# Performance work log

Measured on AMD Instinct MI355X. Metric: run time of the kernel, lower is better.

The kernel has to match this reference:

```python
import jax, jax.numpy as jnp
import numpy as np

N = 262144          # nodes (divisible by 8 for 3 pooling stages)
E = 4194304         # edges (avg degree 16)
PAD = 6             # 2 extra edge slots per pooling stage
IN = 32
HID = (32, 32, 16)


def gcn_conv(x, W, b, src, dst, w):
    """PyG GCNConv: add self-loops, symmetric norm, x@W, scatter-add, +bias.
    src/dst: padded edge arrays; w: float mask (0 = inactive edge)."""
    n = x.shape[0]
    deg = jax.ops.segment_sum(w, dst, num_segments=n) + 1.0  # +1 self-loop
    dinv = jax.lax.rsqrt(deg)                                 # deg >= 1
    h = x @ W
    norm = dinv[src] * dinv[dst] * w                          # [E+PAD]
    out = jax.ops.segment_sum(norm[:, None] * h[src], dst, num_segments=n)
    out = out + (dinv * dinv)[:, None] * h                    # self-loop term
    return out + b


def graph_max_pool(x, src, dst, w, slot):
    """max over adjacent node pairs; keep edges with both endpoints < n//2;
    append edges (m-1,0) and (0,m-1) in pre-allocated padding slots."""
    n = x.shape[0]
    m = n // 2
    xp = jnp.max(x[: 2 * m].reshape(m, 2, x.shape[1]), axis=1)
    valid = ((src < m) & (dst < m)).astype(w.dtype)
    w = w * valid
    src = src.at[slot].set(m - 1).at[slot + 1].set(0)
    dst = dst.at[slot].set(0).at[slot + 1].set(m - 1)
    w = w.at[slot].set(1.0).at[slot + 1].set(1.0)
    return xp, src, dst, w


def setup_inputs() -> dict:
    key = jax.random.key(0)
    ks = jax.random.split(key, 8)
    x = jax.random.normal(ks[0], (N, IN), dtype=jnp.float32)
    edge_index = jax.random.randint(ks[1], (2, E), 0, N, dtype=jnp.int32)
    def lin(k, fi, fo):
        return jax.random.normal(k, (fi, fo), dtype=jnp.float32) / np.float32(np.sqrt(fi))
    return {
        "x": x,
        "edge_index": edge_index,
        "W1": lin(ks[2], IN, HID[0]), "b1": jnp.zeros((HID[0],), jnp.float32),
        "W2": lin(ks[3], HID[0], HID[1]), "b2": jnp.zeros((HID[1],), jnp.float32),
        "W3": lin(ks[4], HID[1], HID[2]), "b3": jnp.zeros((HID[2],), jnp.float32),
    }


def reference(x, edge_index, W1, b1, W2, b2, W3, b3):
    # fixed-size padded edge list with float validity mask
    src = jnp.concatenate([edge_index[0], jnp.zeros((PAD,), edge_index.dtype)])
    dst = jnp.concatenate([edge_index[1], jnp.zeros((PAD,), edge_index.dtype)])
    w = jnp.concatenate([jnp.ones((E,), jnp.float32), jnp.zeros((PAD,), jnp.float32)])

    h = jax.nn.relu(gcn_conv(x, W1, b1, src, dst, w))
    h, src, dst, w = graph_max_pool(h, src, dst, w, E)
    h = jax.nn.relu(gcn_conv(h, W2, b2, src, dst, w))
    h, src, dst, w = graph_max_pool(h, src, dst, w, E + 2)
    h = jax.nn.relu(gcn_conv(h, W3, b3, src, dst, w))
    latent, src, dst, w = graph_max_pool(h, src, dst, w, E + 4)
    return latent, jnp.stack([src, dst]), w
```

## Files before the change

### kernel.cpp

```cpp
#include <hip/hip_runtime.h>
#include <hip/hip_bf16.h>
#include <stdint.h>

#define N_NODES 262144
#define E_EDGES 4194304
#define EPAD    4194310
#define SRC_OFF 524288
#define DST_OFF (524288 + 4194310)
#define W_OFF   (524288 + 2 * 4194310)
#define CAP2    1064960
#define CAP3    270336

using bf16 = __hip_bfloat16;
typedef float f4v __attribute__((ext_vector_type(4)));
typedef float f2v __attribute__((ext_vector_type(2)));

__device__ __forceinline__ float b2f(unsigned int u) {
    union { unsigned int i; float f; } v; v.i = u << 16; return v.f;
}

__device__ __forceinline__ void pk_atomic_add_raw(bf16* addr, uint32_t data) {
    asm volatile("global_atomic_pk_add_bf16 %0, %1, off" :: "v"(addr), "v"(data) : "memory");
}

__device__ __forceinline__ float dinv_of(const float* __restrict__ deg, int i, int n, int pads) {
    float extra = (pads && (i == 0 || i == n - 1)) ? 1.0f : 0.0f;
    return rsqrtf(deg[i] + 1.0f + extra);
}

__global__ void __launch_bounds__(256) tier_hist_kernel(const int* __restrict__ ei,
        float* __restrict__ out, uint32_t* __restrict__ wc, float* __restrict__ deg1) {
    int t = blockIdx.x * 256 + threadIdx.x;
    int4 s0 = ((const int4*)ei)[2 * t];
    int4 s1 = ((const int4*)ei)[2 * t + 1];
    int4 d0 = ((const int4*)(ei + E_EDGES))[2 * t];
    int4 d1 = ((const int4*)(ei + E_EDGES))[2 * t + 1];

    f4v v;
    v = (f4v){(float)s0.x, (float)s0.y, (float)s0.z, (float)s0.w};
    __builtin_nontemporal_store(v, (f4v*)(out + SRC_OFF) + 2 * t);
    v = (f4v){(float)s1.x, (float)s1.y, (float)s1.z, (float)s1.w};
    __builtin_nontemporal_store(v, (f4v*)(out + SRC_OFF) + 2 * t + 1);
    f2v w2;
    w2 = (f2v){(float)d0.x, (float)d0.y}; __builtin_nontemporal_store(w2, (f2v*)(out + DST_OFF) + 4 * t);
    w2 = (f2v){(float)d0.z, (float)d0.w}; __builtin_nontemporal_store(w2, (f2v*)(out + DST_OFF) + 4 * t + 1);
    w2 = (f2v){(float)d1.x, (float)d1.y}; __builtin_nontemporal_store(w2, (f2v*)(out + DST_OFF) + 4 * t + 2);
    w2 = (f2v){(float)d1.z, (float)d1.w}; __builtin_nontemporal_store(w2, (f2v*)(out + DST_OFF) + 4 * t + 3);
    v = (f4v){(s0.x < 32768 && d0.x < 32768) ? 1.0f : 0.0f,
              (s0.y < 32768 && d0.y < 32768) ? 1.0f : 0.0f,
              (s0.z < 32768 && d0.z < 32768) ? 1.0f : 0.0f,
              (s0.w < 32768 && d0.w < 32768) ? 1.0f : 0.0f};
    __builtin_nontemporal_store(v, (f4v*)(out + W_OFF) + 2 * t);
    v = (f4v){(s1.x < 32768 && d1.x < 32768) ? 1.0f : 0.0f,
              (s1.y < 32768 && d1.y < 32768) ? 1.0f : 0.0f,
              (s1.z < 32768 && d1.z < 32768) ? 1.0f : 0.0f,
              (s1.w < 32768 && d1.w < 32768) ? 1.0f : 0.0f};
    __builtin_nontemporal_store(v, (f4v*)(out + W_OFF) + 2 * t + 1);

    atomicAdd(&deg1[d0.x], 1.0f); atomicAdd(&deg1[d0.y], 1.0f);
    atomicAdd(&deg1[d0.z], 1.0f); atomicAdd(&deg1[d0.w], 1.0f);
    atomicAdd(&deg1[d1.x], 1.0f); atomicAdd(&deg1[d1.y], 1.0f);
    atomicAdd(&deg1[d1.z], 1.0f); atomicAdd(&deg1[d1.w], 1.0f);

    int c3 = 0, c2 = 0;
    int ss[8] = {s0.x, s0.y, s0.z, s0.w, s1.x, s1.y, s1.z, s1.w};
    int dd[8] = {d0.x, d0.y, d0.z, d0.w, d1.x, d1.y, d1.z, d1.w};
#pragma unroll
    for (int j = 0; j < 8; ++j) {
        bool b3  = (ss[j] < 65536) & (dd[j] < 65536);
        bool b23 = (ss[j] < 131072) & (dd[j] < 131072);
        c3 += b3; c2 += (b23 & !b3);
    }
    int pk = c2 | (c3 << 16);
    pk += __shfl_xor(pk, 32); pk += __shfl_xor(pk, 16); pk += __shfl_xor(pk, 8);
    pk += __shfl_xor(pk, 4);  pk += __shfl_xor(pk, 2);  pk += __shfl_xor(pk, 1);
    if ((threadIdx.x & 63) == 0) wc[t >> 6] = (uint32_t)pk;
}

__global__ void __launch_bounds__(1024) tier_scan_kernel(const uint32_t* __restrict__ wc,
        uint2* __restrict__ wb, uint32_t* __restrict__ tot, float* __restrict__ out) {
    __shared__ uint32_t wt3[16], wt2[16];
    int t = threadIdx.x, lane = t & 63, w = t >> 6;
    uint32_t v[8]; uint32_t s3 = 0, s2 = 0;
#pragma unroll
    for (int j = 0; j < 8; ++j) {
        v[j] = wc[t * 8 + j];
        s2 += v[j] & 0xFFFFu; s3 += v[j] >> 16;
    }
    uint32_t i3 = s3, i2 = s2;
    for (int off = 1; off < 64; off <<= 1) {
        uint32_t o3 = __shfl_up(i3, off);
        uint32_t o2 = __shfl_up(i2, off);
        if (lane >= off) { i3 += o3; i2 += o2; }
    }
    if (lane == 63) { wt3[w] = i3; wt2[w] = i2; }
    __syncthreads();
    uint32_t wb3 = 0, wb2 = 0;
#pragma unroll
    for (int k = 0; k < 16; ++k) {
        uint32_t m = (k < w) ? 1u : 0u;
        wb3 += m * wt3[k]; wb2 += m * wt2[k];
    }
    uint32_t r3 = wb3 + i3 - s3, r2 = wb2 + i2 - s2;
#pragma unroll
    for (int j = 0; j < 8; ++j) {
        wb[t * 8 + j] = make_uint2(r3, r2);
        r2 += v[j] & 0xFFFFu; r3 += v[j] >> 16;
    }
    if (t == 1023) { tot[0] = wb3 + i3; tot[1] = wb2 + i2; }
    if (t < 6) {
        int stage = t >> 1, m = 131072 >> stage;
        int s, d;
        if ((t & 1) == 0) { s = m - 1; d = 0; } else { s = 0; d = m - 1; }
        int e = E_EDGES + t;
        out[SRC_OFF + e] = (float)s;
        out[DST_OFF + e] = (float)d;
        out[W_OFF + e]   = (stage == 2) ? 1.0f : 0.0f;
    }
}

__global__ void __launch_bounds__(256) compact_kernel(const int* __restrict__ ei,
        const uint2* __restrict__ wb, const uint32_t* __restrict__ tot,
        int2* __restrict__ el, float* __restrict__ deg2, float* __restrict__ deg3) {
    int t = blockIdx.x * 256 + threadIdx.x;
    int lane = threadIdx.x & 63;
    int4 s0 = ((const int4*)ei)[2 * t];
    int4 s1 = ((const int4*)ei)[2 * t + 1];
    int4 d0 = ((const int4*)(ei + E_EDGES))[2 * t];
    int4 d1 = ((const int4*)(ei + E_EDGES))[2 * t + 1];
    uint2 base = wb[t >> 6];
    uint32_t r3 = base.x, r2 = tot[0] + base.y;
    uint64_t lt = (1ull << lane) - 1ull;
    int ss[8] = {s0.x, s0.y, s0.z, s0.w, s1.x, s1.y, s1.z, s1.w};
    int dd[8] = {d0.x, d0.y, d0.z, d0.w, d1.x, d1.y, d1.z, d1.w};
#pragma unroll
    for (int j = 0; j < 8; ++j) {
        int s = ss[j], d = dd[j];
        bool b3  = (s < 65536) & (d < 65536);
        bool b23 = (s < 131072) & (d < 131072);
        bool b2  = b23 & !b3;
        uint64_t m3 = __ballot(b3), m2 = __ballot(b2);
        if (b3) {
            el[r3 + (uint32_t)__popcll(m3 & lt)] = make_int2(s, d);
            atomicAdd(&deg3[d], 1.0f);
        }
        if (b2) {
            uint32_t p = r2 + (uint32_t)__popcll(m2 & lt);
            if (p < CAP2) el[p] = make_int2(s, d);
        }
        if (b23) atomicAdd(&deg2[d], 1.0f);
        r3 += (uint32_t)__popcll(m3); r2 += (uint32_t)__popcll(m2);
    }
}

__global__ void __launch_bounds__(256) xform1_kernel(const float* __restrict__ xin,
        const float* __restrict__ W, const float* __restrict__ deg1,
        bf16* __restrict__ hs, bf16* __restrict__ agg) {
    constexpr int FIN = 32, FOUT = 32, NPB = 8;
    __shared__ float sW[FIN * FOUT];
    __shared__ float sx[NPB * FIN];
    int tid = threadIdx.x;
    for (int i = tid; i < FIN * FOUT; i += 256) sW[i] = W[i];
    int node0 = blockIdx.x * NPB;
    for (int i = tid; i < NPB * FIN; i += 256) sx[i] = xin[node0 * FIN + i];
    __syncthreads();
    int nl = tid / FOUT, j = tid % FOUT;
    int node = node0 + nl;
    float acc = 0.0f;
#pragma unroll
    for (int k = 0; k < FIN; ++k) acc += sx[nl * FIN + k] * sW[k * FOUT + j];
    bf16 v = __float2bfloat16(rsqrtf(deg1[node] + 1.0f) * acc);
    hs[node * FOUT + j]  = v;
    agg[node * FOUT + j] = v;
}

template <int FOUT>
__global__ void __launch_bounds__(256) xform_pool_kernel(const bf16* __restrict__ aggp,
        const float* __restrict__ degp, int prevN, int prevPads, const float* __restrict__ biasp,
        const float* __restrict__ W, const float* __restrict__ deg, int curN,
        bf16* __restrict__ hs, bf16* __restrict__ agg) {
    constexpr int FIN = 32;
    constexpr int NPB = 256 / FOUT;
    __shared__ float sW[FIN * FOUT];
    __shared__ float sx[NPB * FIN];
    const unsigned short* ap = (const unsigned short*)aggp;
    int tid = threadIdx.x;
    for (int i = tid; i < FIN * FOUT; i += 256) sW[i] = W[i];
    int node0 = blockIdx.x * NPB;
    for (int i = tid; i < NPB * FIN; i += 256) {
        int nl = i / FIN, k = i % FIN;
        int g0 = 2 * (node0 + nl);
        float bb = biasp[k];
        float v0 = dinv_of(degp, g0,     prevN, prevPads) * b2f(ap[(size_t)g0 * FIN + k])       + bb;
        float v1 = dinv_of(degp, g0 + 1, prevN, prevPads) * b2f(ap[(size_t)(g0 + 1) * FIN + k]) + bb;
        sx[i] = fmaxf(fmaxf(v0, v1), 0.0f);
    }
    __syncthreads();
    int nl = tid / FOUT, j = tid % FOUT;
    int node = node0 + nl;
    float acc = 0.0f;
#pragma unroll
    for (int k = 0; k < FIN; ++k) acc += sx[nl * FIN + k] * sW[k * FOUT + j];
    bf16 v = __float2bfloat16(dinv_of(deg, node, curN, 1) * acc);
    hs[node * FOUT + j]  = v;
    agg[node * FOUT + j] = v;
}

__global__ void __launch_bounds__(256) scatter1_kernel(const int* __restrict__ ei,
        const bf16* __restrict__ hs, bf16* __restrict__ agg) {
    unsigned idx = blockIdx.x * 256u + threadIdx.x;
    int e = (int)(idx >> 4), p = (int)(idx & 15u);
    int s = ei[e], d = ei[E_EDGES + e];
    uint32_t hw = *(const uint32_t*)((const unsigned short*)hs + (size_t)s * 32 + 2 * p);
    pk_atomic_add_raw(agg + (size_t)d * 32 + 2 * p, hw);
}

template <int FOUT>
__global__ void __launch_bounds__(256) scatter_cmp_kernel(const int2* __restrict__ el,
        const uint32_t* __restrict__ tot, int useN3only,
        const bf16* __restrict__ hs, bf16* __restrict__ agg, int n) {
    constexpr int L = FOUT / 2;
    unsigned idx = blockIdx.x * 256u + threadIdx.x;
    unsigned e = idx / L; int p = (int)(idx % L);
    uint32_t K = useN3only ? tot[0] : (tot[0] + tot[1]);
    if (e >= K + 2) return;
    int s, d;
    if (e < K)       { int2 sd = el[e]; s = sd.x; d = sd.y; }
    else if (e == K) { s = n - 1; d = 0; }
    else             { s = 0;     d = n - 1; }
    uint32_t hw = *(const uint32_t*)((const unsigned short*)hs + (size_t)s * FOUT + 2 * p);
    pk_atomic_add_raw(agg + (size_t)d * FOUT + 2 * p, hw);
}

__global__ void __launch_bounds__(256) pool_out_kernel(const bf16* __restrict__ agg,
        const float* __restrict__ deg3, const float* __restrict__ bias,
        float* __restrict__ outp) {
    unsigned idx = blockIdx.x * 256u + threadIdx.x;
    int i = (int)(idx >> 4), f = (int)(idx & 15);
    int g0 = 2 * i;
    float bb = bias[f];
    float v0 = dinv_of(deg3, g0,     65536, 1) * __bfloat162float(agg[(size_t)g0 * 16 + f])       + bb;
    float v1 = dinv_of(deg3, g0 + 1, 65536, 1) * __bfloat162float(agg[(size_t)(g0 + 1) * 16 + f]) + bb;
    outp[idx] = fmaxf(fmaxf(v0, v1), 0.0f);
}

extern "C" void kernel_launch(void* const* d_in, const int* in_sizes, int n_in,
                              void* d_out, int out_size, void* d_ws, size_t ws_size,
                              hipStream_t stream) {
    const float* x  = (const float*)d_in[0];
    const int*   ei = (const int*)d_in[1];
    const float* W1 = (const float*)d_in[2];
    const float* b1 = (const float*)d_in[3];
    const float* W2 = (const float*)d_in[4];
    const float* b2 = (const float*)d_in[5];
    const float* W3 = (const float*)d_in[6];
    const float* b3 = (const float*)d_in[7];
    float* out = (float*)d_out;

    char* ws = (char*)d_ws;
    bf16*     agg   = (bf16*)ws;
    bf16*     hs    = (bf16*)(ws + (16u << 20));
    int2*     el    = (int2*)(ws + (44u << 20));
    float*    deg1  = (float*)(ws + (55u << 20));
    float*    deg2  = (float*)(ws + (56u << 20));
    float*    deg3  = (float*)(ws + (56u << 20) + (512u << 10));
    uint32_t* wcnt  = (uint32_t*)(ws + (59u << 20));
    uint2*    wbase = (uint2*)(ws + (59u << 20) + (256u << 10));
    uint32_t* totb  = (uint32_t*)(ws + (59u << 20) + (768u << 10));

    hipMemsetAsync(deg1, 0, (1u << 20) + (768u << 10), stream);
    tier_hist_kernel<<<2048, 256, 0, stream>>>(ei, out, wcnt, deg1);
    tier_scan_kernel<<<1, 1024, 0, stream>>>(wcnt, wbase, totb, out);
    compact_kernel<<<2048, 256, 0, stream>>>(ei, wbase, totb, el, deg2, deg3);

    xform1_kernel<<<N_NODES / 8, 256, 0, stream>>>(x, W1, deg1, hs, agg);
    scatter1_kernel<<<E_EDGES * 16 / 256, 256, 0, stream>>>(ei, hs, agg);

    xform_pool_kernel<32><<<131072 / 8, 256, 0, stream>>>(agg, deg1, 262144, 0, b1,
                                                          W2, deg2, 131072, hs, agg);
    scatter_cmp_kernel<32><<<(int)(((unsigned)(CAP2 + 2) * 16 + 255) / 256), 256, 0, stream>>>(
        el, totb, 0, hs, agg, 131072);

    xform_pool_kernel<16><<<65536 / 16, 256, 0, stream>>>(agg, deg2, 131072, 1, b2,
                                                          W3, deg3, 65536, hs, agg);
    scatter_cmp_kernel<16><<<(int)(((unsigned)(CAP3 + 2) * 8 + 255) / 256), 256, 0, stream>>>(
        el, totb, 1, hs, agg, 65536);

    pool_out_kernel<<<32768 * 16 / 256, 256, 0, stream>>>(agg, deg3, b3, out);
}
```

Measured before the change: 644.1 us.

## Replace hist/scan/compact with single-pass segmented atomic compaction, move output writes into scatter1

New measurement: 688.2 us. +6.8%, slower.

```diff
diff --git a/kernel.cpp b/kernel.cpp
--- a/kernel.cpp
+++ b/kernel.cpp
@@ -4,12 +4,16 @@
 
 #define N_NODES 262144
 #define E_EDGES 4194304
-#define EPAD    4194310
 #define SRC_OFF 524288
 #define DST_OFF (524288 + 4194310)
 #define W_OFF   (524288 + 2 * 4194310)
-#define CAP2    1064960
-#define CAP3    270336
+#define NSEG    64
+#define SEG3    4608
+#define SEG2X   13568
+#define T3      (NSEG * SEG3)
+#define T2X     (NSEG * SEG2X)
+#define SCAT1_BLOCKS (E_EDGES * 16 / 256)
+#define OUT_BLOCKS   (E_EDGES / 8 / 256)
 
 using bf16 = __hip_bfloat16;
 typedef float f4v __attribute__((ext_vector_type(4)));
@@ -28,43 +32,26 @@
     return rsqrtf(deg[i] + 1.0f + extra);
 }
 
-__global__ void __launch_bounds__(256) tier_hist_kernel(const int* __restrict__ ei,
-        float* __restrict__ out, uint32_t* __restrict__ wc, float* __restrict__ deg1) {
+__global__ void __launch_bounds__(256) prep_kernel(const int* __restrict__ ei,
+        uint32_t* __restrict__ el3, int2* __restrict__ el2,
+        uint32_t* __restrict__ cnt3, uint32_t* __restrict__ cnt2,
+        float* __restrict__ deg1, float* __restrict__ deg2, float* __restrict__ deg3) {
     int t = blockIdx.x * 256 + threadIdx.x;
+    int lane = threadIdx.x & 63;
+    int seg = (t >> 6) & (NSEG - 1);
     int4 s0 = ((const int4*)ei)[2 * t];
     int4 s1 = ((const int4*)ei)[2 * t + 1];
     int4 d0 = ((const int4*)(ei + E_EDGES))[2 * t];
     int4 d1 = ((const int4*)(ei + E_EDGES))[2 * t + 1];
 
-    f4v v;
-    v = (f4v){(float)s0.x, (float)s0.y, (float)s0.z, (float)s0.w};
-    __builtin_nontemporal_store(v, (f4v*)(out + SRC_OFF) + 2 * t);
-    v = (f4v){(float)s1.x, (float)s1.y, (float)s1.z, (float)s1.w};
-    __builtin_nontemporal_store(v, (f4v*)(out + SRC_OFF) + 2 * t + 1);
-    f2v w2;
-    w2 = (f2v){(float)d0.x, (float)d0.y}; __builtin_nontemporal_store(w2, (f2v*)(out + DST_OFF) + 4 * t);
-    w2 = (f2v){(float)d0.z, (float)d0.w}; __builtin_nontemporal_store(w2, (f2v*)(out + DST_OFF) + 4 * t + 1);
-    w2 = (f2v){(float)d1.x, (float)d1.y}; __builtin_nontemporal_store(w2, (f2v*)(out + DST_OFF) + 4 * t + 2);
-    w2 = (f2v){(float)d1.z, (float)d1.w}; __builtin_nontemporal_store(w2, (f2v*)(out + DST_OFF) + 4 * t + 3);
-    v = (f4v){(s0.x < 32768 && d0.x < 32768) ? 1.0f : 0.0f,
-              (s0.y < 32768 && d0.y < 32768) ? 1.0f : 0.0f,
-              (s0.z < 32768 && d0.z < 32768) ? 1.0f : 0.0f,
-              (s0.w < 32768 && d0.w < 32768) ? 1.0f : 0.0f};
-    __builtin_nontemporal_store(v, (f4v*)(out + W_OFF) + 2 * t);
-    v = (f4v){(s1.x < 32768 && d1.x < 32768) ? 1.0f : 0.0f,
-              (s1.y < 32768 && d1.y < 32768) ? 1.0f : 0.0f,
-              (s1.z < 32768 && d1.z < 32768) ? 1.0f : 0.0f,
-              (s1.w < 32768 && d1.w < 32768) ? 1.0f : 0.0f};
-    __builtin_nontemporal_store(v, (f4v*)(out + W_OFF) + 2 * t + 1);
-
     atomicAdd(&deg1[d0.x], 1.0f); atomicAdd(&deg1[d0.y], 1.0f);
     atomicAdd(&deg1[d0.z], 1.0f); atomicAdd(&deg1[d0.w], 1.0f);
     atomicAdd(&deg1[d1.x], 1.0f); atomicAdd(&deg1[d1.y], 1.0f);
     atomicAdd(&deg1[d1.z], 1.0f); atomicAdd(&deg1[d1.w], 1.0f);
 
-    int c3 = 0, c2 = 0;
     int ss[8] = {s0.x, s0.y, s0.z, s0.w, s1.x, s1.y, s1.z, s1.w};
     int dd[8] = {d0.x, d0.y, d0.z, d0.w, d1.x, d1.y, d1.z, d1.w};
+    int c3 = 0, c2 = 0;
 #pragma unroll
     for (int j = 0; j < 8; ++j) {
         bool b3  = (ss[j] < 65536) & (dd[j] < 65536);
@@ -74,65 +61,16 @@
     int pk = c2 | (c3 << 16);
     pk += __shfl_xor(pk, 32); pk += __shfl_xor(pk, 16); pk += __shfl_xor(pk, 8);
     pk += __shfl_xor(pk, 4);  pk += __shfl_xor(pk, 2);  pk += __shfl_xor(pk, 1);
-    if ((threadIdx.x & 63) == 0) wc[t >> 6] = (uint32_t)pk;
-}
-
-__global__ void __launch_bounds__(1024) tier_scan_kernel(const uint32_t* __restrict__ wc,
-        uint2* __restrict__ wb, uint32_t* __restrict__ tot, float* __restrict__ out) {
-    __shared__ uint32_t wt3[16], wt2[16];
-    int t = threadIdx.x, lane = t & 63, w = t >> 6;
-    uint32_t v[8]; uint32_t s3 = 0, s2 = 0;
-#pragma unroll
-    for (int j = 0; j < 8; ++j) {
-        v[j] = wc[t * 8 + j];
-        s2 += v[j] & 0xFFFFu; s3 += v[j] >> 16;
-    }
-    uint32_t i3 = s3, i2 = s2;
-    for (int off = 1; off < 64; off <<= 1) {
-        uint32_t o3 = __shfl_up(i3, off);
-        uint32_t o2 = __shfl_up(i2, off);
-        if (lane >= off) { i3 += o3; i2 += o2; }
-    }
-    if (lane == 63) { wt3[w] = i3; wt2[w] = i2; }
-    __syncthreads();
-    uint32_t wb3 = 0, wb2 = 0;
-#pragma unroll
-    for (int k = 0; k < 16; ++k) {
-        uint32_t m = (k < w) ? 1u : 0u;
-        wb3 += m * wt3[k]; wb2 += m * wt2[k];
-    }
-    uint32_t r3 = wb3 + i3 - s3, r2 = wb2 + i2 - s2;
-#pragma unroll
-    for (int j = 0; j < 8; ++j) {
-        wb[t * 8 + j] = make_uint2(r3, r2);
-        r2 += v[j] & 0xFFFFu; r3 += v[j] >> 16;
-    }
-    if (t == 1023) { tot[0] = wb3 + i3; tot[1] = wb2 + i2; }
-    if (t < 6) {
-        int stage = t >> 1, m = 131072 >> stage;
-        int s, d;
-        if ((t & 1) == 0) { s = m - 1; d = 0; } else { s = 0; d = m - 1; }
-        int e = E_EDGES + t;
-        out[SRC_OFF + e] = (float)s;
-        out[DST_OFF + e] = (float)d;
-        out[W_OFF + e]   = (stage == 2) ? 1.0f : 0.0f;
-    }
-}
-
-__global__ void __launch_bounds__(256) compact_kernel(const int* __restrict__ ei,
-        const uint2* __restrict__ wb, const uint32_t* __restrict__ tot,
-        int2* __restrict__ el, float* __restrict__ deg2, float* __restrict__ deg3) {
-    int t = blockIdx.x * 256 + threadIdx.x;
-    int lane = threadIdx.x & 63;
-    int4 s0 = ((const int4*)ei)[2 * t];
-    int4 s1 = ((const int4*)ei)[2 * t + 1];
-    int4 d0 = ((const int4*)(ei + E_EDGES))[2 * t];
-    int4 d1 = ((const int4*)(ei + E_EDGES))[2 * t + 1];
-    uint2 base = wb[t >> 6];
-    uint32_t r3 = base.x, r2 = tot[0] + base.y;
+    uint32_t wt2 = (uint32_t)pk & 0xFFFFu, wt3 = (uint32_t)pk >> 16;
+    uint32_t b3base = 0, b2base = 0;
+    if (lane == 0) {
+        b3base = atomicAdd(&cnt3[seg], wt3);
+        b2base = atomicAdd(&cnt2[seg], wt2);
+    }
+    b3base = __shfl(b3base, 0, 64);
+    b2base = __shfl(b2base, 0, 64);
+    uint32_t r3 = b3base, r2 = b2base;
     uint64_t lt = (1ull << lane) - 1ull;
-    int ss[8] = {s0.x, s0.y, s0.z, s0.w, s1.x, s1.y, s1.z, s1.w};
-    int dd[8] = {d0.x, d0.y, d0.z, d0.w, d1.x, d1.y, d1.z, d1.w};
 #pragma unroll
     for (int j = 0; j < 8; ++j) {
         int s = ss[j], d = dd[j];
@@ -141,12 +79,13 @@
         bool b2  = b23 & !b3;
         uint64_t m3 = __ballot(b3), m2 = __ballot(b2);
         if (b3) {
-            el[r3 + (uint32_t)__popcll(m3 & lt)] = make_int2(s, d);
+            uint32_t pos = r3 + (uint32_t)__popcll(m3 & lt);
+            if (pos < SEG3) el3[seg * SEG3 + pos] = (uint32_t)s | ((uint32_t)d << 16);
             atomicAdd(&deg3[d], 1.0f);
         }
         if (b2) {
-            uint32_t p = r2 + (uint32_t)__popcll(m2 & lt);
-            if (p < CAP2) el[p] = make_int2(s, d);
+            uint32_t pos = r2 + (uint32_t)__popcll(m2 & lt);
+            if (pos < SEG2X) el2[seg * SEG2X + pos] = make_int2(s, d);
         }
         if (b23) atomicAdd(&deg2[d], 1.0f);
         r3 += (uint32_t)__popcll(m3); r2 += (uint32_t)__popcll(m2);
@@ -207,7 +146,45 @@
 }
 
 __global__ void __launch_bounds__(256) scatter1_kernel(const int* __restrict__ ei,
-        const bf16* __restrict__ hs, bf16* __restrict__ agg) {
+        const bf16* __restrict__ hs, bf16* __restrict__ agg, float* __restrict__ out) {
+    if (blockIdx.x >= SCAT1_BLOCKS) {
+        int t = (blockIdx.x - SCAT1_BLOCKS) * 256 + threadIdx.x;
+        int4 s0 = ((const int4*)ei)[2 * t];
+        int4 s1 = ((const int4*)ei)[2 * t + 1];
+        int4 d0 = ((const int4*)(ei + E_EDGES))[2 * t];
+        int4 d1 = ((const int4*)(ei + E_EDGES))[2 * t + 1];
+        f4v v;
+        v = (f4v){(float)s0.x, (float)s0.y, (float)s0.z, (float)s0.w};
+        __builtin_nontemporal_store(v, (f4v*)(out + SRC_OFF) + 2 * t);
+        v = (f4v){(float)s1.x, (float)s1.y, (float)s1.z, (float)s1.w};
+        __builtin_nontemporal_store(v, (f4v*)(out + SRC_OFF) + 2 * t + 1);
+        f2v w2;
+        w2 = (f2v){(float)d0.x, (float)d0.y}; __builtin_nontemporal_store(w2, (f2v*)(out + DST_OFF) + 4 * t);
+        w2 = (f2v){(float)d0.z, (float)d0.w}; __builtin_nontemporal_store(w2, (f2v*)(out + DST_OFF) + 4 * t + 1);
+        w2 = (f2v){(float)d1.x, (float)d1.y}; __builtin_nontemporal_store(w2, (f2v*)(out + DST_OFF) + 4 * t + 2);
+        w2 = (f2v){(float)d1.z, (float)d1.w}; __builtin_nontemporal_store(w2, (f2v*)(out + DST_OFF) + 4 * t + 3);
+        v = (f4v){(s0.x < 32768 && d0.x < 32768) ? 1.0f : 0.0f,
+                  (s0.y < 32768 && d0.y < 32768) ? 1.0f : 0.0f,
+                  (s0.z < 32768 && d0.z < 32768) ? 1.0f : 0.0f,
+                  (s0.w < 32768 && d0.w < 32768) ? 1.0f : 0.0f};
+        __builtin_nontemporal_store(v, (f4v*)(out + W_OFF) + 2 * t);
+        v = (f4v){(s1.x < 32768 && d1.x < 32768) ? 1.0f : 0.0f,
+                  (s1.y < 32768 && d1.y < 32768) ? 1.0f : 0.0f,
+                  (s1.z < 32768 && d1.z < 32768) ? 1.0f : 0.0f,
+                  (s1.w < 32768 && d1.w < 32768) ? 1.0f : 0.0f};
+        __builtin_nontemporal_store(v, (f4v*)(out + W_OFF) + 2 * t + 1);
+        if (blockIdx.x == SCAT1_BLOCKS && threadIdx.x < 6) {
+            int k = threadIdx.x;
+            int stage = k >> 1, m = 131072 >> stage;
+            int s, d;
+            if ((k & 1) == 0) { s = m - 1; d = 0; } else { s = 0; d = m - 1; }
+            int e = E_EDGES + k;
+            out[SRC_OFF + e] = (float)s;
+            out[DST_OFF + e] = (float)d;
+            out[W_OFF + e]   = (stage == 2) ? 1.0f : 0.0f;
+        }
+        return;
+    }
     unsigned idx = blockIdx.x * 256u + threadIdx.x;
     int e = (int)(idx >> 4), p = (int)(idx & 15u);
     int s = ei[e], d = ei[E_EDGES + e];
@@ -215,21 +192,45 @@
     pk_atomic_add_raw(agg + (size_t)d * 32 + 2 * p, hw);
 }
 
-template <int FOUT>
-__global__ void __launch_bounds__(256) scatter_cmp_kernel(const int2* __restrict__ el,
-        const uint32_t* __restrict__ tot, int useN3only,
-        const bf16* __restrict__ hs, bf16* __restrict__ agg, int n) {
-    constexpr int L = FOUT / 2;
-    unsigned idx = blockIdx.x * 256u + threadIdx.x;
-    unsigned e = idx / L; int p = (int)(idx % L);
-    uint32_t K = useN3only ? tot[0] : (tot[0] + tot[1]);
-    if (e >= K + 2) return;
+__global__ void __launch_bounds__(256) scatter2_kernel(const uint32_t* __restrict__ el3,
+        const int2* __restrict__ el2, const uint32_t* __restrict__ cnt3,
+        const uint32_t* __restrict__ cnt2, const bf16* __restrict__ hs,
+        bf16* __restrict__ agg) {
+    unsigned idx = blockIdx.x * 256u + threadIdx.x;
+    unsigned e = idx >> 4; int p = (int)(idx & 15u);
     int s, d;
-    if (e < K)       { int2 sd = el[e]; s = sd.x; d = sd.y; }
-    else if (e == K) { s = n - 1; d = 0; }
-    else             { s = 0;     d = n - 1; }
-    uint32_t hw = *(const uint32_t*)((const unsigned short*)hs + (size_t)s * FOUT + 2 * p);
-    pk_atomic_add_raw(agg + (size_t)d * FOUT + 2 * p, hw);
+    if (e < T3) {
+        unsigned seg = e / SEG3, loc = e - seg * SEG3;
+        if (loc >= cnt3[seg]) return;
+        uint32_t v = el3[e];
+        s = (int)(v & 0xFFFFu); d = (int)(v >> 16);
+    } else if (e < T3 + T2X) {
+        unsigned e2 = e - T3, seg = e2 / SEG2X, loc = e2 - seg * SEG2X;
+        if (loc >= cnt2[seg]) return;
+        int2 sd = el2[e2]; s = sd.x; d = sd.y;
+    } else if (e == T3 + T2X)     { s = 131071; d = 0; }
+    else if (e == T3 + T2X + 1)   { s = 0; d = 131071; }
+    else return;
+    uint32_t hw = *(const uint32_t*)((const unsigned short*)hs + (size_t)s * 32 + 2 * p);
+    pk_atomic_add_raw(agg + (size_t)d * 32 + 2 * p, hw);
+}
+
+__global__ void __launch_bounds__(256) scatter3_kernel(const uint32_t* __restrict__ el3,
+        const uint32_t* __restrict__ cnt3, const bf16* __restrict__ hs,
+        bf16* __restrict__ agg) {
+    unsigned idx = blockIdx.x * 256u + threadIdx.x;
+    unsigned e = idx >> 3; int p = (int)(idx & 7u);
+    int s, d;
+    if (e < T3) {
+        unsigned seg = e / SEG3, loc = e - seg * SEG3;
+        if (loc >= cnt3[seg]) return;
+        uint32_t v = el3[e];
+        s = (int)(v & 0xFFFFu); d = (int)(v >> 16);
+    } else if (e == T3)     { s = 65535; d = 0; }
+    else if (e == T3 + 1)   { s = 0; d = 65535; }
+    else return;
+    uint32_t hw = *(const uint32_t*)((const unsigned short*)hs + (size_t)s * 16 + 2 * p);
+    pk_atomic_add_raw(agg + (size_t)d * 16 + 2 * p, hw);
 }
 
 __global__ void __launch_bounds__(256) pool_out_kernel(const bf16* __restrict__ agg,
@@ -260,31 +261,30 @@
     char* ws = (char*)d_ws;
     bf16*     agg   = (bf16*)ws;
     bf16*     hs    = (bf16*)(ws + (16u << 20));
-    int2*     el    = (int2*)(ws + (44u << 20));
+    uint32_t* el3   = (uint32_t*)(ws + (44u << 20));
+    int2*     el2   = (int2*)(ws + (46u << 20));
     float*    deg1  = (float*)(ws + (55u << 20));
     float*    deg2  = (float*)(ws + (56u << 20));
     float*    deg3  = (float*)(ws + (56u << 20) + (512u << 10));
-    uint32_t* wcnt  = (uint32_t*)(ws + (59u << 20));
-    uint2*    wbase = (uint2*)(ws + (59u << 20) + (256u << 10));
-    uint32_t* totb  = (uint32_t*)(ws + (59u << 20) + (768u << 10));
-
-    hipMemsetAsync(deg1, 0, (1u << 20) + (768u << 10), stream);
-    tier_hist_kernel<<<2048, 256, 0, stream>>>(ei, out, wcnt, deg1);
-    tier_scan_kernel<<<1, 1024, 0, stream>>>(wcnt, wbase, totb, out);
-    compact_kernel<<<2048, 256, 0, stream>>>(ei, wbase, totb, el, deg2, deg3);
+    uint32_t* cnt3  = (uint32_t*)(ws + (56u << 20) + (768u << 10));
+    uint32_t* cnt2  = cnt3 + NSEG;
+
+    hipMemsetAsync(deg1, 0, (1u << 20) + (768u << 10) + 512u, stream);
+
+    prep_kernel<<<2048, 256, 0, stream>>>(ei, el3, el2, cnt3, cnt2, deg1, deg2, deg3);
 
     xform1_kernel<<<N_NODES / 8, 256, 0, stream>>>(x, W1, deg1, hs, agg);
-    scatter1_kernel<<<E_EDGES * 16 / 256, 256, 0, stream>>>(ei, hs, agg);
+    scatter1_kernel<<<SCAT1_BLOCKS + OUT_BLOCKS, 256, 0, stream>>>(ei, hs, agg, out);
 
     xform_pool_kernel<32><<<131072 / 8, 256, 0, stream>>>(agg, deg1, 262144, 0, b1,
                                                           W2, deg2, 131072, hs, agg);
-    scatter_cmp_kernel<32><<<(int)(((unsigned)(CAP2 + 2) * 16 + 255) / 256), 256, 0, stream>>>(
-        el, totb, 0, hs, agg, 131072);
+    scatter2_kernel<<<(int)((((unsigned)(T3 + T2X + 2)) * 16 + 255) / 256), 256, 0, stream>>>(
+        el3, el2, cnt3, cnt2, hs, agg);
 
     xform_pool_kernel<16><<<65536 / 16, 256, 0, stream>>>(agg, deg2, 131072, 1, b2,
                                                           W3, deg3, 65536, hs, agg);
-    scatter_cmp_kernel<16><<<(int)(((unsigned)(CAP3 + 2) * 8 + 255) / 256), 256, 0, stream>>>(
-        el, totb, 1, hs, agg, 65536);
+    scatter3_kernel<<<(int)((((unsigned)(T3 + 2)) * 8 + 255) / 256), 256, 0, stream>>>(
+        el3, cnt3, hs, agg);
 
     pool_out_kernel<<<32768 * 16 / 256, 256, 0, stream>>>(agg, deg3, b3, out);
 }
```
